# Kernel optimization log

Measured on AMD Instinct MI355X. Metric: run time of the kernel, lower is better.

## Reference

```python
import jax, jax.numpy as jnp
import numpy as np

B, S, D, H = 8, 1024, 512, 12
HS = D // H  # 42 (head_size; 12*42 = 504 concat width, as in the original)


def setup_inputs() -> dict:
    key = jax.random.key(0)
    ks = jax.random.split(key, 12)
    sd = 0.02
    return {
        "embedded_patches": jax.random.normal(ks[0], (B, S, D), dtype=jnp.float32),
        # stacked per-head projections (12 independent Linear(D, HS, bias=False))
        "wk": jax.random.normal(ks[1], (H, D, HS), dtype=jnp.float32) * sd,
        "wq": jax.random.normal(ks[2], (H, D, HS), dtype=jnp.float32) * sd,
        "wv": jax.random.normal(ks[3], (H, D, HS), dtype=jnp.float32) * sd,
        "w_proj": jax.random.normal(ks[4], (H * HS, D), dtype=jnp.float32) * sd,  # [504, 512]
        "b_proj": jnp.zeros((D,), dtype=jnp.float32),
        # shared LayerNorm (same params used for both norms, as in the original)
        "gamma": jnp.ones((D,), dtype=jnp.float32),
        "beta": jnp.zeros((D,), dtype=jnp.float32),
        "w1": jax.random.normal(ks[5], (D, 4 * D), dtype=jnp.float32) * sd,
        "b1": jnp.zeros((4 * D,), dtype=jnp.float32),
        "w2": jax.random.normal(ks[6], (4 * D, D), dtype=jnp.float32) * sd,
        "b2": jnp.zeros((D,), dtype=jnp.float32),
    }


def _layernorm(x, gamma, beta, eps=1e-5):
    mu = jnp.mean(x, axis=-1, keepdims=True)
    var = jnp.var(x, axis=-1, keepdims=True)
    return (x - mu) * jax.lax.rsqrt(var + eps) * gamma + beta


def reference(embedded_patches, wk, wq, wv, w_proj, b_proj, gamma, beta, w1, b1, w2, b2):
    x = embedded_patches
    n1 = _layernorm(x, gamma, beta)
    # per-head projections, vectorized over heads: [B,S,D] x [H,D,E] -> [B,H,S,E]
    q = jnp.einsum('bsd,hde->bhse', n1, wq)
    k = jnp.einsum('bsd,hde->bhse', n1, wk)
    v = jnp.einsum('bsd,hde->bhse', n1, wv)
    scale = HS ** -0.5
    wei = jax.nn.softmax(jnp.einsum('bhse,bhte->bhst', q, k) * scale, axis=-1)
    out = jnp.einsum('bhst,bhte->bhse', wei, v)        # [B,H,S,E]
    out = out.transpose(0, 2, 1, 3).reshape(B, S, H * HS)  # concat heads -> [B,S,504]
    attn = out @ w_proj + b_proj                       # [B,S,D]
    # original quirk: takes batch element 0 and broadcasts against residual
    first_added = attn[0] + x                          # [S,D] + [B,S,D] -> [B,S,D]
    n2 = _layernorm(first_added, gamma, beta)
    h = jax.nn.gelu(n2 @ w1 + b1, approximate=False)   # torch nn.GELU default = exact erf
    ff = h @ w2 + b2
    return ff + first_added
```

## Files before the change

kernel.cpp:

```cpp
#include <hip/hip_runtime.h>
#include <hip/hip_bf16.h>
#include <stdint.h>


typedef unsigned short u16;
typedef __attribute__((ext_vector_type(8))) short short8;
typedef __attribute__((ext_vector_type(4))) float f32x4;

__device__ __forceinline__ u16 f2bf(float f) {
  union { float f; unsigned u; } x; x.f = f;
  return (u16)((x.u + 0x7FFFu + ((x.u >> 16) & 1u)) >> 16);
}
__device__ __forceinline__ float bf2f(u16 u) {
  union { unsigned u; float f; } x; x.u = ((unsigned)u) << 16;
  return x.f;
}

__device__ __forceinline__ void gload_lds16(const u16* g, u16* l) {
  __builtin_amdgcn_global_load_lds(
      (__attribute__((address_space(1))) void*)g,
      (__attribute__((address_space(3))) void*)l, 16, 0, 0);
}

__device__ __forceinline__ float wred_sum(float v) {
#pragma unroll
  for (int off = 32; off > 0; off >>= 1) v += __shfl_xor(v, off, 64);
  return v;
}
__device__ __forceinline__ float wred_max(float v) {
#pragma unroll
  for (int off = 32; off > 0; off >>= 1) v = fmaxf(v, __shfl_xor(v, off, 64));
  return v;
}

__device__ __forceinline__ float gelu_fast(float t) {
  const float p = __builtin_fmaf(0.0356774081f, t * t, 0.7978845608f);
  return t / (1.0f + __expf(-2.0f * t * p));
}

#define MFMA16x16(a, b, c) __builtin_amdgcn_mfma_f32_16x16x32_bf16(a, b, c, 0, 0, 0)

enum { EP_BF16 = 0, EP_PV = 1, EP_F32B = 2, EP_GELU = 3, EP_OUT = 4,
       EP_PART = 5, EP_PVPART = 6 };

template <int EP>
__launch_bounds__(256, 4)
__global__ void gemm2(const u16* __restrict__ A, int lda, long sAz,
                      const u16* __restrict__ Bt, int ldb, long sBz,
                      void* __restrict__ Cv, int ldc, long sCz,
                      int K, const float* __restrict__ bias,
                      const float* __restrict__ aux) {
  __shared__ u16 lA[2][128 * 32];
  __shared__ u16 lB[2][128 * 32];

  const int gx = gridDim.x, gy = gridDim.y;
  const int lin = blockIdx.x + gx * (blockIdx.y + gy * blockIdx.z);
  const int nwg = gx * gy * gridDim.z;
  const int wg = (lin & 7) * (nwg >> 3) + (lin >> 3);
  const int bx = wg % gx;
  const int tmp = wg / gx;
  const int by = tmp % gy;
  const int z = tmp / gy;

  const u16* Ab;
  const u16* Bb;
  if (EP == EP_PVPART) {
    Ab = A + (long)(z >> 2) * sAz + (z & 3) * 256;
    Bb = Bt + (long)(z >> 2) * sBz + (z & 3) * 256;
  } else {
    Ab = A + (long)z * sAz;
    Bb = Bt + (long)z * sBz;
  }
  const int m0 = bx * 128;
  const int n0 = by * 128;
  const int tid = threadIdx.x;
  const int w = tid >> 6;
  const int l = tid & 63;
  const int wr = w >> 1;
  const int wc = w & 1;
  const int NT = K >> 5;

  f32x4 acc[4][4];
#pragma unroll
  for (int i = 0; i < 4; ++i)
#pragma unroll
    for (int j = 0; j < 4; ++j) acc[i][j] = (f32x4){0.f, 0.f, 0.f, 0.f};

  const int srow = w * 32 + (l >> 2);
  const int sk = (l & 3) * 8;
  const u16* ga0 = Ab + (long)(m0 + srow) * lda + sk;
  const u16* ga1 = Ab + (long)(m0 + srow + 16) * lda + sk;
  const u16* gb0 = Bb + (long)(n0 + srow) * ldb + sk;
  const u16* gb1 = Bb + (long)(n0 + srow + 16) * ldb + sk;
  const int dOff = w * 1024;

  const int aoff = (wr * 64 + (l & 15)) * 32 + (l >> 4) * 8;
  const int boff = (wc * 64 + (l & 15)) * 32 + (l >> 4) * 8;

  gload_lds16(ga0, &lA[0][dOff]);
  gload_lds16(ga1, &lA[0][dOff + 512]);
  gload_lds16(gb0, &lB[0][dOff]);
  gload_lds16(gb1, &lB[0][dOff + 512]);
  __syncthreads();

  int buf = 0;
  for (int t = 0; t < NT; ++t) {
    short8 af[4], bfv[4];
#pragma unroll
    for (int mi = 0; mi < 4; ++mi)
      af[mi] = *(const short8*)&lA[buf][aoff + mi * 16 * 32];
#pragma unroll
    for (int ni = 0; ni < 4; ++ni)
      bfv[ni] = *(const short8*)&lB[buf][boff + ni * 16 * 32];
    if (t + 1 < NT) {
      const int k0 = (t + 1) * 32;
      const int nb = buf ^ 1;
      gload_lds16(ga0 + k0, &lA[nb][dOff]);
      gload_lds16(ga1 + k0, &lA[nb][dOff + 512]);
      gload_lds16(gb0 + k0, &lB[nb][dOff]);
      gload_lds16(gb1 + k0, &lB[nb][dOff + 512]);
    }
#pragma unroll
    for (int mi = 0; mi < 4; ++mi)
#pragma unroll
      for (int ni = 0; ni < 4; ++ni)
        acc[mi][ni] = MFMA16x16(af[mi], bfv[ni], acc[mi][ni]);
    __syncthreads();
    buf ^= 1;
  }

  const int rbase = m0 + wr * 64 + (l >> 4) * 4;
  const int cbase = n0 + wc * 64 + (l & 15);
#pragma unroll
  for (int mi = 0; mi < 4; ++mi) {
#pragma unroll
    for (int ni = 0; ni < 4; ++ni) {
#pragma unroll
      for (int j = 0; j < 4; ++j) {
        const int row = rbase + mi * 16 + j;
        const int col = cbase + ni * 16;
        const float v = acc[mi][ni][j];
        if (EP == EP_BF16) {
          ((u16*)Cv)[(long)z * sCz + (long)row * ldc + col] = f2bf(v);
        } else if (EP == EP_PV) {
          if (col < 42) {
            const float iv = aux[z * 1024 + row];
            ((u16*)Cv)[(long)row * ldc + z * 42 + col] = f2bf(v * iv);
          }
        } else if (EP == EP_F32B) {
          ((float*)Cv)[(long)row * ldc + col] = v + bias[col];
        } else if (EP == EP_GELU) {
          ((u16*)Cv)[(long)row * ldc + col] = f2bf(gelu_fast(v + bias[col]));
        } else if (EP == EP_OUT) {
          ((float*)Cv)[(long)row * ldc + col] =
              v + bias[col] + aux[(long)row * ldc + col];
        } else {
          ((float*)Cv)[(long)z * sCz + (long)row * ldc + col] = v;
        }
      }
    }
  }
}

__global__ void combine_mlp2_kernel(const float* __restrict__ p,
                                    const float* __restrict__ fa,
                                    const float* __restrict__ b2,
                                    float* __restrict__ out) {
  const long i = (long)blockIdx.x * 256 + threadIdx.x;
  const f32x4 a = ((const f32x4*)p)[i];
  const f32x4 b = ((const f32x4*)(p + 8192L * 512))[i];
  const f32x4 f = ((const f32x4*)fa)[i];
  const f32x4 bb = ((const f32x4*)b2)[i & 127];
  ((f32x4*)out)[i] = a + b + f + bb;
}

__global__ void combine_pv_kernel(const float* __restrict__ part,
                                  const float* __restrict__ invl,
                                  u16* __restrict__ cat) {
  const int blk = blockIdx.x;
  const int h = blk >> 10;
  const int row = blk & 1023;
  const int e = threadIdx.x;
  if (e >= 42) return;
  const long base = (long)(h * 4) * 131072 + row * 128 + e;
  float v = part[base] + part[base + 131072] + part[base + 2 * 131072] +
            part[base + 3 * 131072];
  cat[(long)row * 512 + h * 42 + e] = f2bf(v * invl[h * 1024 + row]);
}

__global__ void ln1_kernel(const float* __restrict__ x,
                           const float* __restrict__ gamma,
                           const float* __restrict__ beta,
                           u16* __restrict__ n1) {
  __shared__ float red[16];
  const int s = blockIdx.x;
  const int t = threadIdx.x;
  const float* row = x + (long)s * 512;
  const float v0 = row[t];
  const float v1 = row[t + 256];
  float sum = wred_sum(v0 + v1);
  float sq = wred_sum(v0 * v0 + v1 * v1);
  if ((t & 63) == 0) { red[t >> 6] = sum; red[8 + (t >> 6)] = sq; }
  __syncthreads();
  sum = red[0] + red[1] + red[2] + red[3];
  sq = red[8] + red[9] + red[10] + red[11];
  const float mu = sum * (1.0f / 512.0f);
  const float rstd = rsqrtf(sq * (1.0f / 512.0f) - mu * mu + 1e-5f);
  n1[(long)s * 512 + t] = f2bf((v0 - mu) * rstd * gamma[t] + beta[t]);
  n1[(long)s * 512 + t + 256] =
      f2bf((v1 - mu) * rstd * gamma[t + 256] + beta[t + 256]);
}

__global__ void ln2_kernel(const float* __restrict__ x,
                           const float* __restrict__ aproj,
                           const float* __restrict__ gamma,
                           const float* __restrict__ beta,
                           float* __restrict__ fa, u16* __restrict__ n2) {
  __shared__ float red[16];
  const int r = blockIdx.x;
  const int t = threadIdx.x;
  const int s = r & 1023;
  const float* xr = x + (long)r * 512;
  const float* ar = aproj + (long)s * 512;
  const float v0 = xr[t] + ar[t];
  const float v1 = xr[t + 256] + ar[t + 256];
  fa[(long)r * 512 + t] = v0;
  fa[(long)r * 512 + t + 256] = v1;
  float sum = wred_sum(v0 + v1);
  float sq = wred_sum(v0 * v0 + v1 * v1);
  if ((t & 63) == 0) { red[t >> 6] = sum; red[8 + (t >> 6)] = sq; }
  __syncthreads();
  sum = red[0] + red[1] + red[2] + red[3];
  sq = red[8] + red[9] + red[10] + red[11];
  const float mu = sum * (1.0f / 512.0f);
  const float rstd = rsqrtf(sq * (1.0f / 512.0f) - mu * mu + 1e-5f);
  n2[(long)r * 512 + t] = f2bf((v0 - mu) * rstd * gamma[t] + beta[t]);
  n2[(long)r * 512 + t + 256] =
      f2bf((v1 - mu) * rstd * gamma[t + 256] + beta[t + 256]);
}

__global__ void softmax_kernel(u16* __restrict__ SP, float* __restrict__ invl) {
  __shared__ float red[16];
  const long row = blockIdx.x;
  u16* p = SP + row * 1024;
  const int t = threadIdx.x;
  uint2 u = ((const uint2*)p)[t];
  const float s0 = bf2f((u16)(u.x & 0xffff));
  const float s1 = bf2f((u16)(u.x >> 16));
  const float s2 = bf2f((u16)(u.y & 0xffff));
  const float s3 = bf2f((u16)(u.y >> 16));
  float m = wred_max(fmaxf(fmaxf(s0, s1), fmaxf(s2, s3)));
  if ((t & 63) == 0) red[t >> 6] = m;
  __syncthreads();
  m = fmaxf(fmaxf(red[0], red[1]), fmaxf(red[2], red[3]));
  const float e0 = __expf(s0 - m), e1 = __expf(s1 - m);
  const float e2 = __expf(s2 - m), e3 = __expf(s3 - m);
  float sum = wred_sum(e0 + e1 + e2 + e3);
  if ((t & 63) == 0) red[8 + (t >> 6)] = sum;
  __syncthreads();
  sum = red[8] + red[9] + red[10] + red[11];
  if (t == 0) invl[row] = 1.0f / sum;
  uint2 o;
  o.x = (unsigned)f2bf(e0) | ((unsigned)f2bf(e1) << 16);
  o.y = (unsigned)f2bf(e2) | ((unsigned)f2bf(e3) << 16);
  ((uint2*)p)[t] = o;
}

__global__ void prep_qkv_kernel(const float* __restrict__ wq,
                                const float* __restrict__ wk,
                                u16* __restrict__ BtQKV, float scale) {
  const int i = blockIdx.x * 256 + threadIdx.x;
  const int n = i >> 9, d = i & 511;
  const int pq = n / 768;
  const int h = (n % 768) >> 6;
  const int e = n & 63;
  float v = 0.f;
  if (e < 42) {
    v = (pq ? wk : wq)[((long)h * 512 + d) * 42 + e];
    if (!pq) v *= scale;
  }
  BtQKV[i] = f2bf(v);
}
__global__ void prep_wvT_kernel(const float* __restrict__ wv,
                                u16* __restrict__ wvT) {
  const int i = blockIdx.x * 256 + threadIdx.x;
  const int r = i >> 9, d = i & 511;
  const int h = r >> 7, e = r & 127;
  wvT[i] = f2bf(e < 42 ? wv[((long)h * 512 + d) * 42 + e] : 0.f);
}

__global__ void transpose_bf16_kernel(const float* __restrict__ in,
                                      u16* __restrict__ out, int N, int Kin,
                                      int Kpad) {
  __shared__ float tile[64][65];
  const int n0 = blockIdx.x * 64;
  const int k0 = blockIdx.y * 64;
  const int t = threadIdx.x;
  const int tc = t & 63;
  const int tr = t >> 6;
#pragma unroll
  for (int r = 0; r < 16; ++r) {
    const int kr = tr * 16 + r;
    const int kg = k0 + kr;
    tile[kr][tc] = (kg < Kin) ? in[(long)kg * N + n0 + tc] : 0.f;
  }
  __syncthreads();
  const int nr0 = t >> 4;
  const int kc = (t & 15) * 4;
#pragma unroll
  for (int p = 0; p < 4; ++p) {
    const int nr = nr0 + p * 16;
    ushort4 v;
    v.x = f2bf(tile[kc + 0][nr]);
    v.y = f2bf(tile[kc + 1][nr]);
    v.z = f2bf(tile[kc + 2][nr]);
    v.w = f2bf(tile[kc + 3][nr]);
    *(ushort4*)&out[(long)(n0 + nr) * Kpad + k0 + kc] = v;
  }
}

__global__ void zero_u16_kernel(u16* __restrict__ p) {
  p[blockIdx.x * 256 + threadIdx.x] = 0;
}

extern "C" void kernel_launch(void* const* d_in, const int* in_sizes, int n_in,
                              void* d_out, int out_size, void* d_ws,
                              size_t ws_size, hipStream_t stream) {
  const float* x = (const float*)d_in[0];
  const float* wk = (const float*)d_in[1];
  const float* wq = (const float*)d_in[2];
  const float* wv = (const float*)d_in[3];
  const float* w_proj = (const float*)d_in[4];
  const float* b_proj = (const float*)d_in[5];
  const float* gamma = (const float*)d_in[6];
  const float* beta = (const float*)d_in[7];
  const float* w1 = (const float*)d_in[8];
  const float* b1 = (const float*)d_in[9];
  const float* w2 = (const float*)d_in[10];
  const float* b2 = (const float*)d_in[11];

  char* base = (char*)d_ws;
  size_t off = 0;
  auto alloc = [&](size_t bytes) -> void* {
    void* p = base + off;
    off += (bytes + 255) & ~(size_t)255;
    return p;
  };
  u16* n1 = (u16*)alloc(1024L * 512 * 2);
  u16* qkvc = (u16*)alloc(1024L * 1536 * 2);
  u16* SP = (u16*)alloc(12L * 1024 * 1024 * 2);
  u16* wvT = (u16*)alloc(1536L * 512 * 2);
  u16* vt = (u16*)alloc(1536L * 1024 * 2);
  u16* cat = (u16*)alloc(1024L * 512 * 2);
  float* aproj = (float*)alloc(1024L * 512 * 4);
  float* fa = (float*)alloc(8192L * 512 * 4);
  u16* n2 = (u16*)alloc(8192L * 512 * 2);
  u16* hbuf = (u16*)alloc(8192L * 2048 * 2);
  u16* BtQKV = (u16*)alloc(1536L * 512 * 2);
  u16* BtP = (u16*)alloc(512L * 512 * 2);
  u16* Bt1 = (u16*)alloc(2048L * 512 * 2);
  u16* Bt2 = (u16*)alloc(512L * 2048 * 2);
  float* invl = (float*)alloc(12L * 1024 * 4);
  float* pvpart = (float*)alloc(48L * 1024 * 128 * 4);
  float* part = (float*)d_ws;
  (void)ws_size; (void)in_sizes; (void)n_in; (void)out_size;

  const float scale = 0.15430334996209191f;

  prep_qkv_kernel<<<3072, 256, 0, stream>>>(wq, wk, BtQKV, scale);
  prep_wvT_kernel<<<3072, 256, 0, stream>>>(wv, wvT);
  transpose_bf16_kernel<<<dim3(8, 8), 256, 0, stream>>>(w_proj, BtP, 512, 504, 512);
  transpose_bf16_kernel<<<dim3(32, 8), 256, 0, stream>>>(w1, Bt1, 2048, 512, 512);
  transpose_bf16_kernel<<<dim3(8, 32), 256, 0, stream>>>(w2, Bt2, 512, 2048, 2048);
  zero_u16_kernel<<<2048, 256, 0, stream>>>(cat);
  ln1_kernel<<<1024, 256, 0, stream>>>(x, gamma, beta, n1);

  gemm2<EP_BF16><<<dim3(8, 12, 1), 256, 0, stream>>>(
      n1, 512, 0, BtQKV, 512, 0, qkvc, 1536, 0, 512, nullptr, nullptr);
  gemm2<EP_BF16><<<dim3(12, 8, 1), 256, 0, stream>>>(
      wvT, 512, 0, n1, 512, 0, vt, 1024, 0, 512, nullptr, nullptr);
  gemm2<EP_BF16><<<dim3(8, 8, 12), 256, 0, stream>>>(
      qkvc, 1536, 64, qkvc + 768, 1536, 64, SP, 1024, 1024L * 1024, 64,
      nullptr, nullptr);
  softmax_kernel<<<12288, 256, 0, stream>>>(SP, invl);
  gemm2<EP_PVPART><<<dim3(8, 1, 48), 256, 0, stream>>>(
      SP, 1024, 1024L * 1024, vt, 1024, 128L * 1024, pvpart, 128,
      1024L * 128, 256, nullptr, nullptr);
  combine_pv_kernel<<<12288, 64, 0, stream>>>(pvpart, invl, cat);
  gemm2<EP_F32B><<<dim3(8, 4, 1), 256, 0, stream>>>(
      cat, 512, 0, BtP, 512, 0, aproj, 512, 0, 512, b_proj, nullptr);
  ln2_kernel<<<8192, 256, 0, stream>>>(x, aproj, gamma, beta, fa, n2);
  gemm2<EP_GELU><<<dim3(64, 16, 1), 256, 0, stream>>>(
      n2, 512, 0, Bt1, 512, 0, hbuf, 2048, 0, 512, b1, nullptr);
  gemm2<EP_PART><<<dim3(64, 4, 2), 256, 0, stream>>>(
      hbuf, 2048, 1024, Bt2, 2048, 1024, part, 512, 8192L * 512, 1024,
      nullptr, nullptr);
  combine_mlp2_kernel<<<4096, 256, 0, stream>>>(part, fa, b2, (float*)d_out);
}
```

Baseline: 187.9 us.

## Fuse prep kernels, atomically accumulate MLP2 split-K into pre-initialized output

All weight-prep, zeroing and LN1 kernels are merged into one block-indexed launch, which cuts the number of small kernel launches. LN2 now writes the residual plus b2 directly into the output. The split-K MLP2 GEMM then atomicAdds its partial sums into that output, so the partial buffer and the combine kernel go away. combine_pv is repacked to use full 256-thread blocks instead of 64-thread blocks with idle lanes. The trade-off is scattered per-element float atomics with non-deterministic summation order, and fa is still written even though nothing reads it anymore.

```diff
diff --git a/kernel.cpp b/kernel.cpp
--- a/kernel.cpp
+++ b/kernel.cpp
@@ -40,8 +40,7 @@
 
 #define MFMA16x16(a, b, c) __builtin_amdgcn_mfma_f32_16x16x32_bf16(a, b, c, 0, 0, 0)
 
-enum { EP_BF16 = 0, EP_PV = 1, EP_F32B = 2, EP_GELU = 3, EP_OUT = 4,
-       EP_PART = 5, EP_PVPART = 6 };
+enum { EP_BF16 = 0, EP_F32B = 2, EP_GELU = 3, EP_PVPART = 6, EP_ATOM = 7 };
 
 template <int EP>
 __launch_bounds__(256, 4)
@@ -142,80 +141,130 @@
         const float v = acc[mi][ni][j];
         if (EP == EP_BF16) {
           ((u16*)Cv)[(long)z * sCz + (long)row * ldc + col] = f2bf(v);
-        } else if (EP == EP_PV) {
-          if (col < 42) {
-            const float iv = aux[z * 1024 + row];
-            ((u16*)Cv)[(long)row * ldc + z * 42 + col] = f2bf(v * iv);
-          }
         } else if (EP == EP_F32B) {
           ((float*)Cv)[(long)row * ldc + col] = v + bias[col];
         } else if (EP == EP_GELU) {
           ((u16*)Cv)[(long)row * ldc + col] = f2bf(gelu_fast(v + bias[col]));
-        } else if (EP == EP_OUT) {
-          ((float*)Cv)[(long)row * ldc + col] =
-              v + bias[col] + aux[(long)row * ldc + col];
+        } else if (EP == EP_PVPART) {
+          ((float*)Cv)[(long)z * sCz + (long)row * ldc + col] = v;
         } else {
-          ((float*)Cv)[(long)z * sCz + (long)row * ldc + col] = v;
+          atomicAdd(&((float*)Cv)[(long)row * ldc + col], v);
         }
       }
     }
   }
 }
 
-__global__ void combine_mlp2_kernel(const float* __restrict__ p,
-                                    const float* __restrict__ fa,
-                                    const float* __restrict__ b2,
-                                    float* __restrict__ out) {
-  const long i = (long)blockIdx.x * 256 + threadIdx.x;
-  const f32x4 a = ((const f32x4*)p)[i];
-  const f32x4 b = ((const f32x4*)(p + 8192L * 512))[i];
-  const f32x4 f = ((const f32x4*)fa)[i];
-  const f32x4 bb = ((const f32x4*)b2)[i & 127];
-  ((f32x4*)out)[i] = a + b + f + bb;
-}
-
 __global__ void combine_pv_kernel(const float* __restrict__ part,
                                   const float* __restrict__ invl,
                                   u16* __restrict__ cat) {
-  const int blk = blockIdx.x;
-  const int h = blk >> 10;
-  const int row = blk & 1023;
-  const int e = threadIdx.x;
-  if (e >= 42) return;
+  const int i = blockIdx.x * 256 + threadIdx.x;
+  const int e = i % 42;
+  const int rowh = i / 42;
+  const int row = rowh & 1023;
+  const int h = rowh >> 10;
   const long base = (long)(h * 4) * 131072 + row * 128 + e;
   float v = part[base] + part[base + 131072] + part[base + 2 * 131072] +
             part[base + 3 * 131072];
   cat[(long)row * 512 + h * 42 + e] = f2bf(v * invl[h * 1024 + row]);
 }
 
-__global__ void ln1_kernel(const float* __restrict__ x,
+__device__ __forceinline__ void transpose_body(const float* __restrict__ in,
+                                               u16* __restrict__ out, int N,
+                                               int Kin, int Kpad, int blk,
+                                               int gx, int t, float* smem) {
+  const int n0 = (blk % gx) * 64;
+  const int k0 = (blk / gx) * 64;
+  const int tc = t & 63;
+  const int tr = t >> 6;
+#pragma unroll
+  for (int r = 0; r < 16; ++r) {
+    const int kr = tr * 16 + r;
+    const int kg = k0 + kr;
+    smem[kr * 65 + tc] = (kg < Kin) ? in[(long)kg * N + n0 + tc] : 0.f;
+  }
+  __syncthreads();
+  const int nr0 = t >> 4;
+  const int kc = (t & 15) * 4;
+#pragma unroll
+  for (int p = 0; p < 4; ++p) {
+    const int nr = nr0 + p * 16;
+    ushort4 v;
+    v.x = f2bf(smem[(kc + 0) * 65 + nr]);
+    v.y = f2bf(smem[(kc + 1) * 65 + nr]);
+    v.z = f2bf(smem[(kc + 2) * 65 + nr]);
+    v.w = f2bf(smem[(kc + 3) * 65 + nr]);
+    *(ushort4*)&out[(long)(n0 + nr) * Kpad + k0 + kc] = v;
+  }
+}
+
+__global__ void prep_fused(const float* __restrict__ wq,
+                           const float* __restrict__ wk,
+                           const float* __restrict__ wv,
+                           const float* __restrict__ w_proj,
+                           const float* __restrict__ w1,
+                           const float* __restrict__ w2,
+                           const float* __restrict__ x,
                            const float* __restrict__ gamma,
                            const float* __restrict__ beta,
-                           u16* __restrict__ n1) {
-  __shared__ float red[16];
-  const int s = blockIdx.x;
+                           u16* __restrict__ BtQKV, u16* __restrict__ wvT,
+                           u16* __restrict__ BtP, u16* __restrict__ Bt1,
+                           u16* __restrict__ Bt2, u16* __restrict__ cat,
+                           u16* __restrict__ n1, float scale) {
+  __shared__ float smem[64 * 65];
+  const int blk = blockIdx.x;
   const int t = threadIdx.x;
-  const float* row = x + (long)s * 512;
-  const float v0 = row[t];
-  const float v1 = row[t + 256];
-  float sum = wred_sum(v0 + v1);
-  float sq = wred_sum(v0 * v0 + v1 * v1);
-  if ((t & 63) == 0) { red[t >> 6] = sum; red[8 + (t >> 6)] = sq; }
-  __syncthreads();
-  sum = red[0] + red[1] + red[2] + red[3];
-  sq = red[8] + red[9] + red[10] + red[11];
-  const float mu = sum * (1.0f / 512.0f);
-  const float rstd = rsqrtf(sq * (1.0f / 512.0f) - mu * mu + 1e-5f);
-  n1[(long)s * 512 + t] = f2bf((v0 - mu) * rstd * gamma[t] + beta[t]);
-  n1[(long)s * 512 + t + 256] =
-      f2bf((v1 - mu) * rstd * gamma[t + 256] + beta[t + 256]);
+  if (blk < 3072) {
+    const int i = blk * 256 + t;
+    const int n = i >> 9, d = i & 511;
+    const int pq = n / 768;
+    const int h = (n % 768) >> 6;
+    const int e = n & 63;
+    float v = 0.f;
+    if (e < 42) {
+      v = (pq ? wk : wq)[((long)h * 512 + d) * 42 + e];
+      if (!pq) v *= scale;
+    }
+    BtQKV[i] = f2bf(v);
+  } else if (blk < 6144) {
+    const int i = (blk - 3072) * 256 + t;
+    const int r = i >> 9, d = i & 511;
+    const int h = r >> 7, e = r & 127;
+    wvT[i] = f2bf(e < 42 ? wv[((long)h * 512 + d) * 42 + e] : 0.f);
+  } else if (blk < 6208) {
+    transpose_body(w_proj, BtP, 512, 504, 512, blk - 6144, 8, t, smem);
+  } else if (blk < 6464) {
+    transpose_body(w1, Bt1, 2048, 512, 512, blk - 6208, 32, t, smem);
+  } else if (blk < 6720) {
+    transpose_body(w2, Bt2, 512, 2048, 2048, blk - 6464, 8, t, smem);
+  } else if (blk < 8768) {
+    cat[(blk - 6720) * 256 + t] = 0;
+  } else {
+    const int s = blk - 8768;
+    const float* row = x + (long)s * 512;
+    const float v0 = row[t];
+    const float v1 = row[t + 256];
+    float sum = wred_sum(v0 + v1);
+    float sq = wred_sum(v0 * v0 + v1 * v1);
+    if ((t & 63) == 0) { smem[t >> 6] = sum; smem[8 + (t >> 6)] = sq; }
+    __syncthreads();
+    sum = smem[0] + smem[1] + smem[2] + smem[3];
+    sq = smem[8] + smem[9] + smem[10] + smem[11];
+    const float mu = sum * (1.0f / 512.0f);
+    const float rstd = rsqrtf(sq * (1.0f / 512.0f) - mu * mu + 1e-5f);
+    n1[(long)s * 512 + t] = f2bf((v0 - mu) * rstd * gamma[t] + beta[t]);
+    n1[(long)s * 512 + t + 256] =
+        f2bf((v1 - mu) * rstd * gamma[t + 256] + beta[t + 256]);
+  }
 }
 
 __global__ void ln2_kernel(const float* __restrict__ x,
                            const float* __restrict__ aproj,
                            const float* __restrict__ gamma,
                            const float* __restrict__ beta,
-                           float* __restrict__ fa, u16* __restrict__ n2) {
+                           const float* __restrict__ b2,
+                           float* __restrict__ fa, u16* __restrict__ n2,
+                           float* __restrict__ outp) {
   __shared__ float red[16];
   const int r = blockIdx.x;
   const int t = threadIdx.x;
@@ -226,6 +275,8 @@
   const float v1 = xr[t + 256] + ar[t + 256];
   fa[(long)r * 512 + t] = v0;
   fa[(long)r * 512 + t + 256] = v1;
+  outp[(long)r * 512 + t] = v0 + b2[t];
+  outp[(long)r * 512 + t + 256] = v1 + b2[t + 256];
   float sum = wred_sum(v0 + v1);
   float sq = wred_sum(v0 * v0 + v1 * v1);
   if ((t & 63) == 0) { red[t >> 6] = sum; red[8 + (t >> 6)] = sq; }
@@ -264,63 +315,6 @@
   o.x = (unsigned)f2bf(e0) | ((unsigned)f2bf(e1) << 16);
   o.y = (unsigned)f2bf(e2) | ((unsigned)f2bf(e3) << 16);
   ((uint2*)p)[t] = o;
-}
-
-__global__ void prep_qkv_kernel(const float* __restrict__ wq,
-                                const float* __restrict__ wk,
-                                u16* __restrict__ BtQKV, float scale) {
-  const int i = blockIdx.x * 256 + threadIdx.x;
-  const int n = i >> 9, d = i & 511;
-  const int pq = n / 768;
-  const int h = (n % 768) >> 6;
-  const int e = n & 63;
-  float v = 0.f;
-  if (e < 42) {
-    v = (pq ? wk : wq)[((long)h * 512 + d) * 42 + e];
-    if (!pq) v *= scale;
-  }
-  BtQKV[i] = f2bf(v);
-}
-__global__ void prep_wvT_kernel(const float* __restrict__ wv,
-                                u16* __restrict__ wvT) {
-  const int i = blockIdx.x * 256 + threadIdx.x;
-  const int r = i >> 9, d = i & 511;
-  const int h = r >> 7, e = r & 127;
-  wvT[i] = f2bf(e < 42 ? wv[((long)h * 512 + d) * 42 + e] : 0.f);
-}
-
-__global__ void transpose_bf16_kernel(const float* __restrict__ in,
-                                      u16* __restrict__ out, int N, int Kin,
-                                      int Kpad) {
-  __shared__ float tile[64][65];
-  const int n0 = blockIdx.x * 64;
-  const int k0 = blockIdx.y * 64;
-  const int t = threadIdx.x;
-  const int tc = t & 63;
-  const int tr = t >> 6;
-#pragma unroll
-  for (int r = 0; r < 16; ++r) {
-    const int kr = tr * 16 + r;
-    const int kg = k0 + kr;
-    tile[kr][tc] = (kg < Kin) ? in[(long)kg * N + n0 + tc] : 0.f;
-  }
-  __syncthreads();
-  const int nr0 = t >> 4;
-  const int kc = (t & 15) * 4;
-#pragma unroll
-  for (int p = 0; p < 4; ++p) {
-    const int nr = nr0 + p * 16;
-    ushort4 v;
-    v.x = f2bf(tile[kc + 0][nr]);
-    v.y = f2bf(tile[kc + 1][nr]);
-    v.z = f2bf(tile[kc + 2][nr]);
-    v.w = f2bf(tile[kc + 3][nr]);
-    *(ushort4*)&out[(long)(n0 + nr) * Kpad + k0 + kc] = v;
-  }
-}
-
-__global__ void zero_u16_kernel(u16* __restrict__ p) {
-  p[blockIdx.x * 256 + threadIdx.x] = 0;
 }
 
 extern "C" void kernel_launch(void* const* d_in, const int* in_sizes, int n_in,
@@ -362,18 +356,13 @@
   u16* Bt2 = (u16*)alloc(512L * 2048 * 2);
   float* invl = (float*)alloc(12L * 1024 * 4);
   float* pvpart = (float*)alloc(48L * 1024 * 128 * 4);
-  float* part = (float*)d_ws;
   (void)ws_size; (void)in_sizes; (void)n_in; (void)out_size;
 
   const float scale = 0.15430334996209191f;
 
-  prep_qkv_kernel<<<3072, 256, 0, stream>>>(wq, wk, BtQKV, scale);
-  prep_wvT_kernel<<<3072, 256, 0, stream>>>(wv, wvT);
-  transpose_bf16_kernel<<<dim3(8, 8), 256, 0, stream>>>(w_proj, BtP, 512, 504, 512);
-  transpose_bf16_kernel<<<dim3(32, 8), 256, 0, stream>>>(w1, Bt1, 2048, 512, 512);
-  transpose_bf16_kernel<<<dim3(8, 32), 256, 0, stream>>>(w2, Bt2, 512, 2048, 2048);
-  zero_u16_kernel<<<2048, 256, 0, stream>>>(cat);
-  ln1_kernel<<<1024, 256, 0, stream>>>(x, gamma, beta, n1);
+  prep_fused<<<9792, 256, 0, stream>>>(wq, wk, wv, w_proj, w1, w2, x, gamma,
+                                       beta, BtQKV, wvT, BtP, Bt1, Bt2, cat,
+                                       n1, scale);
 
   gemm2<EP_BF16><<<dim3(8, 12, 1), 256, 0, stream>>>(
       n1, 512, 0, BtQKV, 512, 0, qkvc, 1536, 0, 512, nullptr, nullptr);
@@ -386,14 +375,14 @@
   gemm2<EP_PVPART><<<dim3(8, 1, 48), 256, 0, stream>>>(
       SP, 1024, 1024L * 1024, vt, 1024, 128L * 1024, pvpart, 128,
       1024L * 128, 256, nullptr, nullptr);
-  combine_pv_kernel<<<12288, 64, 0, stream>>>(pvpart, invl, cat);
+  combine_pv_kernel<<<2016, 256, 0, stream>>>(pvpart, invl, cat);
   gemm2<EP_F32B><<<dim3(8, 4, 1), 256, 0, stream>>>(
       cat, 512, 0, BtP, 512, 0, aproj, 512, 0, 512, b_proj, nullptr);
-  ln2_kernel<<<8192, 256, 0, stream>>>(x, aproj, gamma, beta, fa, n2);
+  ln2_kernel<<<8192, 256, 0, stream>>>(x, aproj, gamma, beta, b2, fa, n2,
+                                       (float*)d_out);
   gemm2<EP_GELU><<<dim3(64, 16, 1), 256, 0, stream>>>(
       n2, 512, 0, Bt1, 512, 0, hbuf, 2048, 0, 512, b1, nullptr);
-  gemm2<EP_PART><<<dim3(64, 4, 2), 256, 0, stream>>>(
-      hbuf, 2048, 1024, Bt2, 2048, 1024, part, 512, 8192L * 512, 1024,
-      nullptr, nullptr);
-  combine_mlp2_kernel<<<4096, 256, 0, stream>>>(part, fa, b2, (float*)d_out);
-}
+  gemm2<EP_ATOM><<<dim3(64, 4, 2), 256, 0, stream>>>(
+      hbuf, 2048, 1024, Bt2, 2048, 1024, d_out, 512, 0, 1024, nullptr,
+      nullptr);
+}
```

After: 177.0 us. -5.8%, faster.
